# Kernel tuning notes

Measured on AMD Instinct MI355X. Metric: run time of the kernel, lower is better.

Reference implementation:

```python
import jax, jax.numpy as jnp
import numpy as np

DIM = 1024
HEADS = 16
HEAD_DIM = DIM // HEADS
B, NQ, NK = 2, 2048, 2048


def setup_inputs() -> dict:
    key = jax.random.key(0)
    ks = jax.random.split(key, 8)
    s = 1.0 / np.sqrt(DIM)
    return {
        "query": jax.random.normal(ks[0], (B, NQ, DIM), jnp.float32),
        "key": jax.random.normal(ks[1], (B, NK, DIM), jnp.float32),
        "value": jax.random.normal(ks[2], (B, NK, DIM), jnp.float32),
        "qpos": jnp.zeros((B, NQ), jnp.int32),
        "kpos": jnp.zeros((B, NK), jnp.int32),
        "Wq": jax.random.normal(ks[3], (DIM, DIM), jnp.float32) * s,
        "Wk": jax.random.normal(ks[4], (DIM, DIM), jnp.float32) * s,
        "Wv": jax.random.normal(ks[5], (DIM, DIM), jnp.float32) * s,
        "Wo": jax.random.normal(ks[6], (DIM, DIM), jnp.float32) * s,
        "bo": jax.random.normal(ks[7], (DIM,), jnp.float32) * s,
    }


def reference(query, key, value, qpos, kpos, Wq, Wk, Wv, Wo, bo):
    # torch nn.Linear: y = x @ W.T (qkv_bias=False)
    Bq, Nq, C = query.shape
    Nk = key.shape[1]
    scale = HEAD_DIM ** -0.5
    # project and split heads: (B, H, N, Dh)
    q = (query @ Wq.T).reshape(Bq, Nq, HEADS, HEAD_DIM).transpose(0, 2, 1, 3)
    k = (key @ Wk.T).reshape(Bq, Nk, HEADS, HEAD_DIM).transpose(0, 2, 1, 3)
    v = (value @ Wv.T).reshape(Bq, Nk, HEADS, HEAD_DIM).transpose(0, 2, 1, 3)
    # rope is None, qk_norm False -> plain softmax attention
    attn = jnp.einsum("bhqd,bhkd->bhqk", q, k) * scale  # [B,H,Nq,Nk]
    attn = jax.nn.softmax(attn, axis=-1)
    x = jnp.einsum("bhqk,bhkd->bhqd", attn, v)
    x = x.transpose(0, 2, 1, 3).reshape(Bq, Nq, C)
    return x @ Wo.T + bo
```

## Files before the change

### kernel.cpp

```cpp
#include <hip/hip_runtime.h>
#include <hip/hip_bf16.h>
#include <stdint.h>

typedef __bf16 bf16_t;
typedef __bf16 bf16x4 __attribute__((ext_vector_type(4)));
typedef __bf16 bf16x8 __attribute__((ext_vector_type(8)));
typedef float  f32x4  __attribute__((ext_vector_type(4)));
typedef unsigned u32x2 __attribute__((ext_vector_type(2)));

#define MFMA16(a,b,c) __builtin_amdgcn_mfma_f32_16x16x32_bf16((a),(b),(c),0,0,0)

static constexpr int DIM = 1024, HEADS = 16, HD = 64, NB = 2, NQ = 2048, NKK = 2048;
static constexpr int MROWS = NB * NQ;
static constexpr float SCALE_Q = 0.18033688011112042f;

__global__ void cvt_all(const float* __restrict__ q, const float* __restrict__ k,
                        const float* __restrict__ v, const float* __restrict__ wq,
                        const float* __restrict__ wk, const float* __restrict__ wv,
                        const float* __restrict__ wo,
                        bf16_t* qb, bf16_t* kb, bf16_t* vb,
                        bf16_t* wqb, bf16_t* wkb, bf16_t* wvb, bf16_t* wob) {
  const int seg = blockIdx.y;
  const float* src; bf16_t* dst;
  size_t base;
  if (seg < 12) {
    int t = seg >> 2;
    src = t == 0 ? q : t == 1 ? k : v;
    dst = t == 0 ? qb : t == 1 ? kb : vb;
    base = (size_t)(seg & 3) * 262144;
  } else {
    int t = seg - 12;
    src = t == 0 ? wq : t == 1 ? wk : t == 2 ? wv : wo;
    dst = t == 0 ? wqb : t == 1 ? wkb : t == 2 ? wvb : wob;
    base = 0;
  }
  size_t i = base + blockIdx.x * 256 + threadIdx.x;
  float4 val = reinterpret_cast<const float4*>(src)[i];
  bf16x4 o;
  o[0] = (bf16_t)val.x; o[1] = (bf16_t)val.y; o[2] = (bf16_t)val.z; o[3] = (bf16_t)val.w;
  *reinterpret_cast<bf16x4*>(dst + i * 4) = o;
}

template<int ROWS>
__device__ __forceinline__ void stage_swz(const bf16_t* gbase, int gstride, bf16_t* lds, int tid) {
#pragma unroll
  for (int c = 0; c < ROWS / 32; ++c) {
    int p = c * 256 + tid;
    int r = p >> 3, x = p & 7;
    const bf16_t* src = gbase + (size_t)r * gstride + ((x ^ (r & 7)) << 3);
    __builtin_amdgcn_global_load_lds(
        (const __attribute__((address_space(1))) void*)src,
        (__attribute__((address_space(3))) void*)(lds + (p << 3)),
        16, 0, 0);
  }
}

__device__ __forceinline__ bf16x8 lds_read8_swz(const bf16_t* lds, int row, int chunk) {
  int sc = chunk ^ (row & 7);
  return *reinterpret_cast<const bf16x8*>(lds + row * 64 + (sc << 3));
}

__device__ __forceinline__ unsigned cvtpk_bf16(float lo, float hi) {
  unsigned r;
  asm("v_cvt_pk_bf16_f32 %0, %1, %2" : "=v"(r) : "v"(lo), "v"(hi));
  return r;
}

__global__ __launch_bounds__(256) void gemm_qkv(const bf16_t* __restrict__ qb,
                                                const bf16_t* __restrict__ kb,
                                                const bf16_t* __restrict__ vb,
                                                const bf16_t* __restrict__ Wq,
                                                const bf16_t* __restrict__ Wk,
                                                const bf16_t* __restrict__ Wv,
                                                bf16_t* __restrict__ Qp,
                                                bf16_t* __restrict__ Kp,
                                                bf16_t* __restrict__ Vt) {
  constexpr int K = DIM, N = DIM;
  __shared__ __align__(16) bf16_t As[128 * 64];
  __shared__ __align__(16) bf16_t Bs[128 * 64];
  const int tid = threadIdx.x;
  const int lane = tid & 63, wid = tid >> 6;
  const int l15 = lane & 15, lg = lane >> 4;
  const int wr = wid >> 1, wc = wid & 1;
  const int bn = blockIdx.x, bm = blockIdx.y;
  const int sel = bn >> 3, bnl = bn & 7;

  const bf16_t* A  = sel == 0 ? qb : sel == 1 ? kb : vb;
  const bf16_t* Bt = sel == 0 ? Wq : sel == 1 ? Wk : Wv;
  const bf16_t* Abase = A + (size_t)(bm * 128) * K;
  const bf16_t* Bbase = Bt + (size_t)(bnl * 128) * K;

  f32x4 acc[4][4];
#pragma unroll
  for (int m = 0; m < 4; ++m)
#pragma unroll
    for (int n = 0; n < 4; ++n) acc[m][n] = (f32x4){0.f, 0.f, 0.f, 0.f};

  for (int k0 = 0; k0 < K; k0 += 64) {
    __syncthreads();
    stage_swz<128>(Abase + k0, K, As, tid);
    stage_swz<128>(Bbase + k0, K, Bs, tid);
    __syncthreads();
#pragma unroll
    for (int kk = 0; kk < 2; ++kk) {
      bf16x8 af[4], bfr[4];
#pragma unroll
      for (int m = 0; m < 4; ++m) af[m] = lds_read8_swz(As, wr * 64 + m * 16 + l15, kk * 4 + lg);
#pragma unroll
      for (int n = 0; n < 4; ++n) bfr[n] = lds_read8_swz(Bs, wc * 64 + n * 16 + l15, kk * 4 + lg);
#pragma unroll
      for (int m = 0; m < 4; ++m)
#pragma unroll
        for (int n = 0; n < 4; ++n)
          acc[m][n] = MFMA16(af[m], bfr[n], acc[m][n]);
    }
  }

  if (sel == 2) {
#pragma unroll
    for (int m = 0; m < 4; ++m) {
      int row0 = bm * 128 + wr * 64 + m * 16 + lg * 4;
      int bb = row0 >> 11, kv = row0 & 2047;
#pragma unroll
      for (int n = 0; n < 4; ++n) {
        int col = bnl * 128 + wc * 64 + n * 16 + l15;
        int hh = col >> 6, dd = col & 63;
        bf16x4 pk;
#pragma unroll
        for (int j = 0; j < 4; ++j) pk[j] = (bf16_t)acc[m][n][j];
        *reinterpret_cast<bf16x4*>(Vt + (((size_t)((bb * 16 + hh) * 64 + dd)) << 11) + kv) = pk;
      }
    }
  } else {
    bf16_t* Cout = sel == 0 ? Qp : Kp;
    const float scale = sel == 0 ? SCALE_Q : 1.0f;
#pragma unroll
    for (int m = 0; m < 4; ++m)
#pragma unroll
      for (int n = 0; n < 4; ++n)
#pragma unroll
        for (int j = 0; j < 4; ++j) {
          int row = bm * 128 + wr * 64 + m * 16 + lg * 4 + j;
          int col = bnl * 128 + wc * 64 + n * 16 + l15;
          Cout[(size_t)row * N + col] = (bf16_t)(acc[m][n][j] * scale);
        }
  }
}

__global__ __launch_bounds__(256) void gemm_out(const bf16_t* __restrict__ A,
                                                const bf16_t* __restrict__ Bt,
                                                float* __restrict__ Cout,
                                                const float* __restrict__ bias) {
  constexpr int K = DIM, N = DIM;
  __shared__ __align__(16) bf16_t As[128 * 64];
  __shared__ __align__(16) bf16_t Bs[128 * 64];
  const int tid = threadIdx.x;
  const int lane = tid & 63, wid = tid >> 6;
  const int l15 = lane & 15, lg = lane >> 4;
  const int wr = wid >> 1, wc = wid & 1;
  const int bn = blockIdx.x, bm = blockIdx.y;

  const bf16_t* Abase = A + (size_t)(bm * 128) * K;
  const bf16_t* Bbase = Bt + (size_t)(bn * 128) * K;

  f32x4 acc[4][4];
#pragma unroll
  for (int m = 0; m < 4; ++m)
#pragma unroll
    for (int n = 0; n < 4; ++n) acc[m][n] = (f32x4){0.f, 0.f, 0.f, 0.f};

  for (int k0 = 0; k0 < K; k0 += 64) {
    __syncthreads();
    stage_swz<128>(Abase + k0, K, As, tid);
    stage_swz<128>(Bbase + k0, K, Bs, tid);
    __syncthreads();
#pragma unroll
    for (int kk = 0; kk < 2; ++kk) {
      bf16x8 af[4], bfr[4];
#pragma unroll
      for (int m = 0; m < 4; ++m) af[m] = lds_read8_swz(As, wr * 64 + m * 16 + l15, kk * 4 + lg);
#pragma unroll
      for (int n = 0; n < 4; ++n) bfr[n] = lds_read8_swz(Bs, wc * 64 + n * 16 + l15, kk * 4 + lg);
#pragma unroll
      for (int m = 0; m < 4; ++m)
#pragma unroll
        for (int n = 0; n < 4; ++n)
          acc[m][n] = MFMA16(af[m], bfr[n], acc[m][n]);
    }
  }

#pragma unroll
  for (int m = 0; m < 4; ++m)
#pragma unroll
    for (int n = 0; n < 4; ++n)
#pragma unroll
      for (int j = 0; j < 4; ++j) {
        int row = bm * 128 + wr * 64 + m * 16 + lg * 4 + j;
        int col = bn * 128 + wc * 64 + n * 16 + l15;
        Cout[(size_t)row * N + col] = acc[m][n][j] + bias[col];
      }
}

__global__ __launch_bounds__(256) void attn_fused(const bf16_t* __restrict__ Qp,
                                                  const bf16_t* __restrict__ Kp,
                                                  const bf16_t* __restrict__ Vt,
                                                  bf16_t* __restrict__ Xa) {
  __shared__ __align__(16) bf16_t Ks[2][64 * 64];
  __shared__ __align__(16) bf16_t Vs[2][64 * 64];
  __shared__ __align__(16) bf16_t Ps[4][32 * 64];
  const int tid = threadIdx.x;
  const int lane = tid & 63, wid = tid >> 6;
  const int l15 = lane & 15, lg = lane >> 4;
  const int rot = (l15 & 7) * 8;

  int id = blockIdx.x + 16 * (blockIdx.y + 16 * blockIdx.z);
  int swz = (id & 7) * 64 + (id >> 3);
  const int bx = swz & 15, h = (swz >> 4) & 15, b = swz >> 8;
  const int q0 = bx * 128;

  const bf16_t* qbase = Qp + ((size_t)(b * NQ + q0)) * DIM + h * HD;
  const bf16_t* kbase = Kp + ((size_t)b * NKK) * DIM + h * HD;
  const bf16_t* vbase = Vt + ((size_t)((b * HEADS + h) * HD)) * NKK;

  stage_swz<128>(qbase, DIM, &Ks[0][0], tid);
  __syncthreads();
  bf16x8 qf[2][2];
#pragma unroll
  for (int g = 0; g < 2; ++g) {
    qf[g][0] = lds_read8_swz(&Ks[0][0], wid * 32 + g * 16 + l15, lg);
    qf[g][1] = lds_read8_swz(&Ks[0][0], wid * 32 + g * 16 + l15, 4 + lg);
  }
  __syncthreads();

  float m_[2] = {-1e30f, -1e30f}, l_[2] = {0.f, 0.f};
  f32x4 o[2][4];
#pragma unroll
  for (int g = 0; g < 2; ++g)
#pragma unroll
    for (int n = 0; n < 4; ++n) o[g][n] = (f32x4){0.f, 0.f, 0.f, 0.f};

  stage_swz<64>(kbase, DIM, &Ks[0][0], tid);
  stage_swz<64>(vbase, NKK, &Vs[0][0], tid);
  __syncthreads();

  int cur = 0;
  for (int it = 0; it < NKK / 64; ++it) {
    if (it + 1 < NKK / 64) {
      stage_swz<64>(kbase + (size_t)(it + 1) * 64 * DIM, DIM, &Ks[cur ^ 1][0], tid);
      stage_swz<64>(vbase + (it + 1) * 64, NKK, &Vs[cur ^ 1][0], tid);
    }
    const bf16_t* kl = &Ks[cur][0];
    const bf16_t* vl = &Vs[cur][0];

    bf16x8 kf0[4], kf1[4];
#pragma unroll
    for (int t = 0; t < 4; ++t) {
      kf0[t] = lds_read8_swz(kl, t * 16 + l15, lg);
      kf1[t] = lds_read8_swz(kl, t * 16 + l15, 4 + lg);
    }

    f32x4 s[2][4];
#pragma unroll
    for (int g = 0; g < 2; ++g)
#pragma unroll
      for (int t = 0; t < 4; ++t) s[g][t] = (f32x4){0.f, 0.f, 0.f, 0.f};
    __builtin_amdgcn_s_setprio(1);
#pragma unroll
    for (int g = 0; g < 2; ++g)
#pragma unroll
      for (int t = 0; t < 4; ++t) {
        s[g][t] = MFMA16(kf0[t], qf[g][0], s[g][t]);
        s[g][t] = MFMA16(kf1[t], qf[g][1], s[g][t]);
      }
    __builtin_amdgcn_s_setprio(0);

#pragma unroll
    for (int g = 0; g < 2; ++g) {
      float rm = s[g][0][0];
#pragma unroll
      for (int t = 0; t < 4; ++t)
#pragma unroll
        for (int j = 0; j < 4; ++j) rm = fmaxf(rm, s[g][t][j]);
      rm = fmaxf(rm, __shfl_xor(rm, 16));
      rm = fmaxf(rm, __shfl_xor(rm, 32));
      if (!__all(rm <= m_[g] + 8.f)) {
        float mn = fmaxf(m_[g], rm);
        float al = exp2f(m_[g] - mn);
        m_[g] = mn;
        l_[g] *= al;
#pragma unroll
        for (int n = 0; n < 4; ++n)
#pragma unroll
          for (int j = 0; j < 4; ++j) o[g][n][j] *= al;
      }
      float rs = 0.f;
#pragma unroll
      for (int t = 0; t < 4; ++t)
#pragma unroll
        for (int j = 0; j < 4; ++j) {
          float p = exp2f(s[g][t][j] - m_[g]);
          s[g][t][j] = p;
          rs += p;
        }
      rs += __shfl_xor(rs, 16);
      rs += __shfl_xor(rs, 32);
      l_[g] += rs;
    }

    bf16_t* Pw = &Ps[wid][0];
#pragma unroll
    for (int g = 0; g < 2; ++g)
#pragma unroll
      for (int t = 0; t < 4; ++t) {
        unsigned w0 = cvtpk_bf16(s[g][t][0], s[g][t][1]);
        unsigned w1 = cvtpk_bf16(s[g][t][2], s[g][t][3]);
        int col = (16 * t + 4 * lg + rot) & 63;
        u32x2 pk2 = {w0, w1};
        *reinterpret_cast<u32x2*>(reinterpret_cast<char*>(Pw) + (g * 16 + l15) * 128 + col * 2) = pk2;
      }
    asm volatile("s_waitcnt lgkmcnt(0)" ::: "memory");
    bf16x8 pf[2][2];
#pragma unroll
    for (int g = 0; g < 2; ++g)
#pragma unroll
      for (int kt = 0; kt < 2; ++kt) {
        int col = (32 * kt + 8 * lg + rot) & 63;
        pf[g][kt] = *reinterpret_cast<const bf16x8*>(
            reinterpret_cast<const char*>(Pw) + (g * 16 + l15) * 128 + col * 2);
      }

    __builtin_amdgcn_s_setprio(1);
#pragma unroll
    for (int n = 0; n < 4; ++n) {
      bf16x8 vf0 = lds_read8_swz(vl, n * 16 + l15, lg);
      bf16x8 vf1 = lds_read8_swz(vl, n * 16 + l15, 4 + lg);
#pragma unroll
      for (int g = 0; g < 2; ++g) {
        o[g][n] = MFMA16(vf0, pf[g][0], o[g][n]);
        o[g][n] = MFMA16(vf1, pf[g][1], o[g][n]);
      }
    }
    __builtin_amdgcn_s_setprio(0);

    __syncthreads();
    cur ^= 1;
  }

#pragma unroll
  for (int g = 0; g < 2; ++g) {
    float inv = 1.f / l_[g];
    int q = q0 + wid * 32 + g * 16 + l15;
    bf16_t* ob = Xa + ((size_t)(b * NQ + q)) * DIM + h * HD;
#pragma unroll
    for (int n = 0; n < 4; ++n) {
      bf16x4 pk;
#pragma unroll
      for (int j = 0; j < 4; ++j) pk[j] = (bf16_t)(o[g][n][j] * inv);
      *reinterpret_cast<bf16x4*>(ob + n * 16 + 4 * lg) = pk;
    }
  }
}

extern "C" void kernel_launch(void* const* d_in, const int* in_sizes, int n_in,
                              void* d_out, int out_size, void* d_ws, size_t ws_size,
                              hipStream_t stream) {
  (void)in_sizes; (void)n_in; (void)out_size; (void)ws_size;
  const float* q  = (const float*)d_in[0];
  const float* k  = (const float*)d_in[1];
  const float* v  = (const float*)d_in[2];
  const float* Wq = (const float*)d_in[5];
  const float* Wk = (const float*)d_in[6];
  const float* Wv = (const float*)d_in[7];
  const float* Wo = (const float*)d_in[8];
  const float* bo = (const float*)d_in[9];
  float* out = (float*)d_out;

  bf16_t* ws = (bf16_t*)d_ws;
  const size_t SZ_IN = (size_t)MROWS * DIM;
  const size_t SZ_W  = (size_t)DIM * DIM;
  bf16_t* qb  = ws;
  bf16_t* kb  = qb  + SZ_IN;
  bf16_t* vb  = kb  + SZ_IN;
  bf16_t* wqb = vb  + SZ_IN;
  bf16_t* wkb = wqb + SZ_W;
  bf16_t* wvb = wkb + SZ_W;
  bf16_t* wob = wvb + SZ_W;
  bf16_t* Qp  = wob + SZ_W;
  bf16_t* Kp  = Qp  + SZ_IN;
  bf16_t* Vtp = Kp  + SZ_IN;
  bf16_t* Xa  = qb;

  cvt_all<<<dim3(1024, 16), 256, 0, stream>>>(q, k, v, Wq, Wk, Wv, Wo,
                                              qb, kb, vb, wqb, wkb, wvb, wob);

  gemm_qkv<<<dim3(24, MROWS / 128), 256, 0, stream>>>(qb, kb, vb, wqb, wkb, wvb,
                                                      Qp, Kp, Vtp);

  attn_fused<<<dim3(NQ / 128, HEADS, NB), 256, 0, stream>>>(Qp, Kp, Vtp, Xa);

  gemm_out<<<dim3(DIM / 128, MROWS / 128), 256, 0, stream>>>(Xa, wob, out, bo);
}
```

Before: 170.3 us.

## Shrink attention query tile to 64 and software-pipeline QK^T one tile ahead

The attention kernel now processes 64 query rows per block (16 per wave) instead of 128, which doubles the grid to 1024 blocks. It also restructures the loop so the QK^T MFMAs for the next key tile are issued before the softmax and PV of the current tile. K and V staging use separate ring offsets to support this. The aim is more blocks per CU and overlap of matrix work with the exp/reduction work, at the cost of reloading each K/V tile twice as often across blocks and less register reuse of K/V fragments.

```diff
diff --git a/kernel.cpp b/kernel.cpp
--- a/kernel.cpp
+++ b/kernel.cpp
@@ -207,157 +207,141 @@
                                                   bf16_t* __restrict__ Xa) {
   __shared__ __align__(16) bf16_t Ks[2][64 * 64];
   __shared__ __align__(16) bf16_t Vs[2][64 * 64];
-  __shared__ __align__(16) bf16_t Ps[4][32 * 64];
+  __shared__ __align__(16) bf16_t Ps[4][16 * 64];
   const int tid = threadIdx.x;
   const int lane = tid & 63, wid = tid >> 6;
   const int l15 = lane & 15, lg = lane >> 4;
   const int rot = (l15 & 7) * 8;
 
-  int id = blockIdx.x + 16 * (blockIdx.y + 16 * blockIdx.z);
-  int swz = (id & 7) * 64 + (id >> 3);
-  const int bx = swz & 15, h = (swz >> 4) & 15, b = swz >> 8;
-  const int q0 = bx * 128;
+  int id = blockIdx.x + 32 * (blockIdx.y + 16 * blockIdx.z);
+  int swz = (id & 7) * 128 + (id >> 3);
+  const int bx = swz & 31, h = (swz >> 5) & 15, b = swz >> 9;
+  const int q0 = bx * 64;
 
   const bf16_t* qbase = Qp + ((size_t)(b * NQ + q0)) * DIM + h * HD;
   const bf16_t* kbase = Kp + ((size_t)b * NKK) * DIM + h * HD;
   const bf16_t* vbase = Vt + ((size_t)((b * HEADS + h) * HD)) * NKK;
 
-  stage_swz<128>(qbase, DIM, &Ks[0][0], tid);
+  stage_swz<64>(qbase, DIM, &Ks[0][0], tid);
   __syncthreads();
-  bf16x8 qf[2][2];
-#pragma unroll
-  for (int g = 0; g < 2; ++g) {
-    qf[g][0] = lds_read8_swz(&Ks[0][0], wid * 32 + g * 16 + l15, lg);
-    qf[g][1] = lds_read8_swz(&Ks[0][0], wid * 32 + g * 16 + l15, 4 + lg);
-  }
+  bf16x8 qf[2];
+  qf[0] = lds_read8_swz(&Ks[0][0], wid * 16 + l15, lg);
+  qf[1] = lds_read8_swz(&Ks[0][0], wid * 16 + l15, 4 + lg);
   __syncthreads();
 
-  float m_[2] = {-1e30f, -1e30f}, l_[2] = {0.f, 0.f};
-  f32x4 o[2][4];
-#pragma unroll
-  for (int g = 0; g < 2; ++g)
-#pragma unroll
-    for (int n = 0; n < 4; ++n) o[g][n] = (f32x4){0.f, 0.f, 0.f, 0.f};
+  float m_ = -1e30f, l_ = 0.f;
+  f32x4 o[4];
+#pragma unroll
+  for (int n = 0; n < 4; ++n) o[n] = (f32x4){0.f, 0.f, 0.f, 0.f};
+
+  constexpr int NT = NKK / 64;
+
+#define QK_TILE(kl, sdst)                                              \
+  do {                                                                 \
+    __builtin_amdgcn_s_setprio(1);                                     \
+    _Pragma("unroll")                                                  \
+    for (int tt = 0; tt < 4; ++tt) {                                   \
+      bf16x8 kf0 = lds_read8_swz((kl), tt * 16 + l15, lg);             \
+      bf16x8 kf1 = lds_read8_swz((kl), tt * 16 + l15, 4 + lg);         \
+      f32x4 a = (f32x4){0.f, 0.f, 0.f, 0.f};                           \
+      a = MFMA16(kf0, qf[0], a);                                       \
+      a = MFMA16(kf1, qf[1], a);                                       \
+      (sdst)[tt] = a;                                                  \
+    }                                                                  \
+    __builtin_amdgcn_s_setprio(0);                                     \
+  } while (0)
 
   stage_swz<64>(kbase, DIM, &Ks[0][0], tid);
   stage_swz<64>(vbase, NKK, &Vs[0][0], tid);
   __syncthreads();
-
-  int cur = 0;
-  for (int it = 0; it < NKK / 64; ++it) {
-    if (it + 1 < NKK / 64) {
-      stage_swz<64>(kbase + (size_t)(it + 1) * 64 * DIM, DIM, &Ks[cur ^ 1][0], tid);
-      stage_swz<64>(vbase + (it + 1) * 64, NKK, &Vs[cur ^ 1][0], tid);
-    }
-    const bf16_t* kl = &Ks[cur][0];
-    const bf16_t* vl = &Vs[cur][0];
-
-    bf16x8 kf0[4], kf1[4];
-#pragma unroll
-    for (int t = 0; t < 4; ++t) {
-      kf0[t] = lds_read8_swz(kl, t * 16 + l15, lg);
-      kf1[t] = lds_read8_swz(kl, t * 16 + l15, 4 + lg);
-    }
-
-    f32x4 s[2][4];
-#pragma unroll
-    for (int g = 0; g < 2; ++g)
-#pragma unroll
-      for (int t = 0; t < 4; ++t) s[g][t] = (f32x4){0.f, 0.f, 0.f, 0.f};
+  f32x4 scur[4];
+  QK_TILE(&Ks[0][0], scur);
+  stage_swz<64>(kbase + (size_t)64 * DIM, DIM, &Ks[1][0], tid);
+  __syncthreads();
+
+  for (int t = 0; t < NT; ++t) {
+    if (t + 1 < NT) stage_swz<64>(vbase + (t + 1) * 64, NKK, &Vs[(t + 1) & 1][0], tid);
+    if (t + 2 < NT) stage_swz<64>(kbase + (size_t)(t + 2) * 64 * DIM, DIM, &Ks[t & 1][0], tid);
+
+    f32x4 snx[4];
+    if (t + 1 < NT) QK_TILE(&Ks[(t + 1) & 1][0], snx);
+
+    float rm = scur[0][0];
+#pragma unroll
+    for (int tt = 0; tt < 4; ++tt)
+#pragma unroll
+      for (int j = 0; j < 4; ++j) rm = fmaxf(rm, scur[tt][j]);
+    rm = fmaxf(rm, __shfl_xor(rm, 16));
+    rm = fmaxf(rm, __shfl_xor(rm, 32));
+    if (!__all(rm <= m_ + 8.f)) {
+      float mn = fmaxf(m_, rm);
+      float al = exp2f(m_ - mn);
+      m_ = mn;
+      l_ *= al;
+#pragma unroll
+      for (int n = 0; n < 4; ++n)
+#pragma unroll
+        for (int j = 0; j < 4; ++j) o[n][j] *= al;
+    }
+    float rs = 0.f;
+#pragma unroll
+    for (int tt = 0; tt < 4; ++tt)
+#pragma unroll
+      for (int j = 0; j < 4; ++j) {
+        float p = exp2f(scur[tt][j] - m_);
+        scur[tt][j] = p;
+        rs += p;
+      }
+    rs += __shfl_xor(rs, 16);
+    rs += __shfl_xor(rs, 32);
+    l_ += rs;
+
+    bf16_t* Pw = &Ps[wid][0];
+#pragma unroll
+    for (int tt = 0; tt < 4; ++tt) {
+      unsigned w0 = cvtpk_bf16(scur[tt][0], scur[tt][1]);
+      unsigned w1 = cvtpk_bf16(scur[tt][2], scur[tt][3]);
+      int col = (16 * tt + 4 * lg + rot) & 63;
+      u32x2 pk2 = {w0, w1};
+      *reinterpret_cast<u32x2*>(reinterpret_cast<char*>(Pw) + l15 * 128 + col * 2) = pk2;
+    }
+    asm volatile("s_waitcnt lgkmcnt(0)" ::: "memory");
+    bf16x8 pf[2];
+#pragma unroll
+    for (int kt = 0; kt < 2; ++kt) {
+      int col = (32 * kt + 8 * lg + rot) & 63;
+      pf[kt] = *reinterpret_cast<const bf16x8*>(reinterpret_cast<const char*>(Pw) + l15 * 128 + col * 2);
+    }
+
+    const bf16_t* vl = &Vs[t & 1][0];
     __builtin_amdgcn_s_setprio(1);
 #pragma unroll
-    for (int g = 0; g < 2; ++g)
-#pragma unroll
-      for (int t = 0; t < 4; ++t) {
-        s[g][t] = MFMA16(kf0[t], qf[g][0], s[g][t]);
-        s[g][t] = MFMA16(kf1[t], qf[g][1], s[g][t]);
+    for (int n = 0; n < 4; ++n) {
+#pragma unroll
+      for (int kt = 0; kt < 2; ++kt) {
+        bf16x8 vf = lds_read8_swz(vl, n * 16 + l15, 4 * kt + lg);
+        o[n] = MFMA16(vf, pf[kt], o[n]);
       }
+    }
     __builtin_amdgcn_s_setprio(0);
 
-#pragma unroll
-    for (int g = 0; g < 2; ++g) {
-      float rm = s[g][0][0];
-#pragma unroll
-      for (int t = 0; t < 4; ++t)
-#pragma unroll
-        for (int j = 0; j < 4; ++j) rm = fmaxf(rm, s[g][t][j]);
-      rm = fmaxf(rm, __shfl_xor(rm, 16));
-      rm = fmaxf(rm, __shfl_xor(rm, 32));
-      if (!__all(rm <= m_[g] + 8.f)) {
-        float mn = fmaxf(m_[g], rm);
-        float al = exp2f(m_[g] - mn);
-        m_[g] = mn;
-        l_[g] *= al;
-#pragma unroll
-        for (int n = 0; n < 4; ++n)
-#pragma unroll
-          for (int j = 0; j < 4; ++j) o[g][n][j] *= al;
-      }
-      float rs = 0.f;
-#pragma unroll
-      for (int t = 0; t < 4; ++t)
-#pragma unroll
-        for (int j = 0; j < 4; ++j) {
-          float p = exp2f(s[g][t][j] - m_[g]);
-          s[g][t][j] = p;
-          rs += p;
-        }
-      rs += __shfl_xor(rs, 16);
-      rs += __shfl_xor(rs, 32);
-      l_[g] += rs;
-    }
-
-    bf16_t* Pw = &Ps[wid][0];
-#pragma unroll
-    for (int g = 0; g < 2; ++g)
-#pragma unroll
-      for (int t = 0; t < 4; ++t) {
-        unsigned w0 = cvtpk_bf16(s[g][t][0], s[g][t][1]);
-        unsigned w1 = cvtpk_bf16(s[g][t][2], s[g][t][3]);
-        int col = (16 * t + 4 * lg + rot) & 63;
-        u32x2 pk2 = {w0, w1};
-        *reinterpret_cast<u32x2*>(reinterpret_cast<char*>(Pw) + (g * 16 + l15) * 128 + col * 2) = pk2;
-      }
-    asm volatile("s_waitcnt lgkmcnt(0)" ::: "memory");
-    bf16x8 pf[2][2];
-#pragma unroll
-    for (int g = 0; g < 2; ++g)
-#pragma unroll
-      for (int kt = 0; kt < 2; ++kt) {
-        int col = (32 * kt + 8 * lg + rot) & 63;
-        pf[g][kt] = *reinterpret_cast<const bf16x8*>(
-            reinterpret_cast<const char*>(Pw) + (g * 16 + l15) * 128 + col * 2);
-      }
-
-    __builtin_amdgcn_s_setprio(1);
-#pragma unroll
-    for (int n = 0; n < 4; ++n) {
-      bf16x8 vf0 = lds_read8_swz(vl, n * 16 + l15, lg);
-      bf16x8 vf1 = lds_read8_swz(vl, n * 16 + l15, 4 + lg);
-#pragma unroll
-      for (int g = 0; g < 2; ++g) {
-        o[g][n] = MFMA16(vf0, pf[g][0], o[g][n]);
-        o[g][n] = MFMA16(vf1, pf[g][1], o[g][n]);
-      }
-    }
-    __builtin_amdgcn_s_setprio(0);
-
-    __syncthreads();
-    cur ^= 1;
-  }
-
-#pragma unroll
-  for (int g = 0; g < 2; ++g) {
-    float inv = 1.f / l_[g];
-    int q = q0 + wid * 32 + g * 16 + l15;
-    bf16_t* ob = Xa + ((size_t)(b * NQ + q)) * DIM + h * HD;
-#pragma unroll
-    for (int n = 0; n < 4; ++n) {
-      bf16x4 pk;
-#pragma unroll
-      for (int j = 0; j < 4; ++j) pk[j] = (bf16_t)(o[g][n][j] * inv);
-      *reinterpret_cast<bf16x4*>(ob + n * 16 + 4 * lg) = pk;
-    }
+    __syncthreads();
+    if (t + 1 < NT) {
+#pragma unroll
+      for (int tt = 0; tt < 4; ++tt) scur[tt] = snx[tt];
+    }
+  }
+#undef QK_TILE
+
+  float inv = 1.f / l_;
+  int q = q0 + wid * 16 + l15;
+  bf16_t* ob = Xa + ((size_t)(b * NQ + q)) * DIM + h * HD;
+#pragma unroll
+  for (int n = 0; n < 4; ++n) {
+    bf16x4 pk;
+#pragma unroll
+    for (int j = 0; j < 4; ++j) pk[j] = (bf16_t)(o[n][j] * inv);
+    *reinterpret_cast<bf16x4*>(ob + n * 16 + 4 * lg) = pk;
   }
 }
 
@@ -396,7 +380,7 @@
   gemm_qkv<<<dim3(24, MROWS / 128), 256, 0, stream>>>(qb, kb, vb, wqb, wkb, wvb,
                                                       Qp, Kp, Vtp);
 
-  attn_fused<<<dim3(NQ / 128, HEADS, NB), 256, 0, stream>>>(Qp, Kp, Vtp, Xa);
+  attn_fused<<<dim3(NQ / 64, HEADS, NB), 256, 0, stream>>>(Qp, Kp, Vtp, Xa);
 
   gemm_out<<<dim3(DIM / 128, MROWS / 128), 256, 0, stream>>>(Xa, wob, out, bo);
 }
```

Measured after the change: 164.7 us. 1.03x faster.
